# Kernel tuning notes

Hardware: AMD Instinct MI355X
Metric: run time of the kernel (lower is better)

The kernel has to match this reference:

```python
import jax, jax.numpy as jnp
import numpy as np

DIM = 1024
NUM_HEADS = 16
HEAD_DIM = DIM // NUM_HEADS
B, S = 4, 2048


def setup_inputs() -> dict:
    key = jax.random.key(0)
    ks = jax.random.split(key, 6)
    scale = 1.0 / np.sqrt(DIM)
    x = jax.random.normal(ks[0], (B, S, DIM), dtype=jnp.float32)
    # per-head projection weights, torch Linear layout [out, in] stacked over heads
    Wq = jax.random.normal(ks[1], (NUM_HEADS, HEAD_DIM, DIM), dtype=jnp.float32) * scale
    Wk = jax.random.normal(ks[2], (NUM_HEADS, HEAD_DIM, DIM), dtype=jnp.float32) * scale
    Wv = jax.random.normal(ks[3], (NUM_HEADS, HEAD_DIM, DIM), dtype=jnp.float32) * scale
    Wo = jax.random.normal(ks[4], (DIM, DIM), dtype=jnp.float32) * scale
    bo = jax.random.normal(ks[5], (DIM,), dtype=jnp.float32) * scale
    return {"x": x, "Wq": Wq, "Wk": Wk, "Wv": Wv, "Wo": Wo, "bo": bo}


def reference(x, Wq, Wk, Wv, Wo, bo):
    # q/k/v: [B, H, S, E]  (torch Linear: x @ W.T)
    q = jnp.einsum('bsd,hed->bhse', x, Wq)
    k = jnp.einsum('bsd,hed->bhse', x, Wk)
    v = jnp.einsum('bsd,hed->bhse', x, Wv)
    sm_scale = HEAD_DIM ** -0.5
    scores = jnp.einsum('bhse,bhte->bhst', q, k) * sm_scale  # [B,H,S,S]
    attn = jax.nn.softmax(scores, axis=-1)  # dropout is identity (eval)
    out = jnp.einsum('bhst,bhte->bhse', attn, v)  # [B,H,S,E]
    # concat heads (head order matches torch.cat over ModuleList)
    out = out.transpose(0, 2, 1, 3).reshape(B, S, DIM)
    return out @ Wo.T + bo
```

## Files before the change

kernel.cpp:

```cpp
#include <hip/hip_runtime.h>

typedef unsigned short u16;
typedef unsigned int u32;
typedef __attribute__((ext_vector_type(8))) _Float16 f16x8;
typedef __attribute__((ext_vector_type(4))) _Float16 f16x4;
typedef __attribute__((ext_vector_type(8))) unsigned short u16x8;
typedef __attribute__((ext_vector_type(4))) float f32x4;

#define MFMA16(a, b, c) __builtin_amdgcn_mfma_f32_16x16x32_f16(a, b, c, 0, 0, 0)

#define CEXP 0.18033688011112042f

__device__ __forceinline__ void async_copy16(void* lds, const void* gmem) {
  __builtin_amdgcn_global_load_lds((const __attribute__((address_space(1))) u32*)gmem,
                                   (__attribute__((address_space(3))) u32*)lds, 16, 0, 0);
}

__device__ __forceinline__ u32 pack2(float a, float b) {
  return __builtin_bit_cast(u32, __builtin_amdgcn_cvt_pkrtz(a, b));
}

__global__ void cvt_f32_f16(const float* __restrict__ in, _Float16* __restrict__ out, int n4) {
  int i = blockIdx.x * blockDim.x + threadIdx.x;
  if (i < n4) {
    float4 v = ((const float4*)in)[i];
    f16x4 o = {(_Float16)v.x, (_Float16)v.y, (_Float16)v.z, (_Float16)v.w};
    ((f16x4*)out)[i] = o;
  }
}

__global__ void transpose_v(const u16* __restrict__ V, u16* __restrict__ Vt) {
  const int bh = blockIdx.y;
  const int e = threadIdx.x & 63;
  const int sb = threadIdx.x >> 6;
  const int s0 = blockIdx.x * 32 + sb * 8;
  const u16* src = V + ((size_t)bh * 2048 + s0) * 64 + e;
  u16x8 tmp;
#pragma unroll
  for (int j = 0; j < 8; ++j) tmp[j] = src[j * 64];
  u16* dst = Vt + ((size_t)bh * 64 + e) * 2048 + s0;
  *(u16x8*)dst = tmp;
}

template <int EPI>
__global__ void gemm_bt(const _Float16* __restrict__ A, const _Float16* __restrict__ Bt,
                        int M, int N, int K,
                        _Float16* __restrict__ q_out, _Float16* __restrict__ k_out,
                        _Float16* __restrict__ v_out,
                        float* __restrict__ outf, const float* __restrict__ bias) {
  __shared__ _Float16 As[128 * 32];
  __shared__ _Float16 Bs[128 * 32];
  const int tid = threadIdx.x;
  const int lane = tid & 63, wid = tid >> 6;
  const int g = lane >> 4, fr = lane & 15;
  const int wr = wid >> 1, wc = wid & 1;
  const int m0 = blockIdx.y * 128, n0 = blockIdx.x * 128;
  const int ldr = tid >> 2, ldc = (tid & 3) * 8;

  f32x4 acc[4][4];
#pragma unroll
  for (int i = 0; i < 4; ++i)
#pragma unroll
    for (int j = 0; j < 4; ++j) acc[i][j] = (f32x4){0.f, 0.f, 0.f, 0.f};

  const _Float16* ga = A + (size_t)(m0 + ldr) * K + ldc;
  const _Float16* gb = Bt + (size_t)(n0 + ldr) * K + ldc;

  for (int kt = 0; kt < K; kt += 32) {
    __syncthreads();
    async_copy16(&As[(size_t)tid * 8], ga + kt);
    async_copy16(&As[(size_t)(256 + tid) * 8], ga + (size_t)64 * K + kt);
    async_copy16(&Bs[(size_t)tid * 8], gb + kt);
    async_copy16(&Bs[(size_t)(256 + tid) * 8], gb + (size_t)64 * K + kt);
    __syncthreads();
    f16x8 af[4], bf[4];
#pragma unroll
    for (int i = 0; i < 4; ++i) af[i] = *(const f16x8*)&As[(wr * 64 + i * 16 + fr) * 32 + g * 8];
#pragma unroll
    for (int j = 0; j < 4; ++j) bf[j] = *(const f16x8*)&Bs[(wc * 64 + j * 16 + fr) * 32 + g * 8];
#pragma unroll
    for (int i = 0; i < 4; ++i)
#pragma unroll
      for (int j = 0; j < 4; ++j) acc[i][j] = MFMA16(af[i], bf[j], acc[i][j]);
  }

#pragma unroll
  for (int i = 0; i < 4; ++i) {
#pragma unroll
    for (int j = 0; j < 4; ++j) {
      const int rb = m0 + wr * 64 + i * 16 + g * 4;
      const int c = n0 + wc * 64 + j * 16 + fr;
      if (EPI == 0) {
        const int which = c >> 10, nn = c & 1023;
        const int h = nn >> 6, e = nn & 63;
        _Float16* dst = (which == 0) ? q_out : (which == 1) ? k_out : v_out;
#pragma unroll
        for (int r = 0; r < 4; ++r) {
          const int row = rb + r, b = row >> 11, s = row & 2047;
          dst[(((size_t)(b * 16 + h)) * 2048 + s) * 64 + e] = (_Float16)acc[i][j][r];
        }
      } else {
#pragma unroll
        for (int r = 0; r < 4; ++r) {
          const int row = rb + r;
          outf[(size_t)row * N + c] = acc[i][j][r] + bias[c];
        }
      }
    }
  }
}

__global__ __launch_bounds__(256, 4)
void attn_kernel(const _Float16* __restrict__ Q, const _Float16* __restrict__ K,
                 const _Float16* __restrict__ Vt, _Float16* __restrict__ AO) {
  __shared__ _Float16 Ks[64 * 64];
  __shared__ _Float16 Vs[64 * 64];
  const int tid = threadIdx.x;
  const int bh = blockIdx.y;
  const int wid = tid >> 6, lane = tid & 63;
  const int g = lane >> 4, q = lane & 15;
  const int qs = q & 7;

  const int qbase = blockIdx.x * 128 + wid * 32;
  const _Float16* Qp0 = Q + ((size_t)bh * 2048 + qbase + q) * 64;
  f16x8 qf[2][2];
  qf[0][0] = *(const f16x8*)(Qp0 + g * 8);
  qf[0][1] = *(const f16x8*)(Qp0 + 32 + g * 8);
  qf[1][0] = *(const f16x8*)(Qp0 + 16 * 64 + g * 8);
  qf[1][1] = *(const f16x8*)(Qp0 + 16 * 64 + 32 + g * 8);

  const int srow = tid >> 3;
  const int sslot = (tid & 7) ^ (srow & 7);
  const _Float16* ksrc = K + (size_t)bh * 131072 + (size_t)srow * 64 + sslot * 8;
  const _Float16* vsrc = Vt + (size_t)bh * 131072 + (size_t)srow * 2048 + sslot * 8;

  f32x4 o[2][4];
#pragma unroll
  for (int qg = 0; qg < 2; ++qg)
#pragma unroll
    for (int t = 0; t < 4; ++t) o[qg][t] = (f32x4){0.f, 0.f, 0.f, 0.f};
  float m[2] = {-1e30f, -1e30f}, l[2] = {0.f, 0.f};

  for (int s0 = 0; s0 < 2048; s0 += 64) {
    __syncthreads();
    async_copy16(&Ks[(size_t)tid * 8], ksrc + (size_t)s0 * 64);
    async_copy16(&Ks[(size_t)(256 + tid) * 8], ksrc + (size_t)(s0 + 32) * 64);
    async_copy16(&Vs[(size_t)tid * 8], vsrc + s0);
    async_copy16(&Vs[(size_t)(256 + tid) * 8], vsrc + (size_t)32 * 2048 + s0);
    __syncthreads();

    const f32x4 z = {0.f, 0.f, 0.f, 0.f};
    f32x4 st[2][4];
#pragma unroll
    for (int kg = 0; kg < 4; ++kg) {
      const int row = kg * 16 + q;
      const f16x8 ka0 = *(const f16x8*)&Ks[row * 64 + ((g ^ qs) << 3)];
      const f16x8 ka1 = *(const f16x8*)&Ks[row * 64 + ((((g + 4)) ^ qs) << 3)];
      st[0][kg] = MFMA16(ka0, qf[0][0], z);
      st[0][kg] = MFMA16(ka1, qf[0][1], st[0][kg]);
      st[1][kg] = MFMA16(ka0, qf[1][0], z);
      st[1][kg] = MFMA16(ka1, qf[1][1], st[1][kg]);
    }

    u32 pk[2][8];
    float scl[2];
#pragma unroll
    for (int qg = 0; qg < 2; ++qg) {
      float cmax = -1e30f;
#pragma unroll
      for (int kg = 0; kg < 4; ++kg)
#pragma unroll
        for (int r = 0; r < 4; ++r) cmax = fmaxf(cmax, st[qg][kg][r]);
      cmax = fmaxf(cmax, __shfl_xor(cmax, 16));
      cmax = fmaxf(cmax, __shfl_xor(cmax, 32));
      const float mnew = fmaxf(m[qg], cmax);
      scl[qg] = __builtin_amdgcn_exp2f((m[qg] - mnew) * CEXP);
      float psum = 0.f;
#pragma unroll
      for (int kg = 0; kg < 4; ++kg) {
        float p0 = __builtin_amdgcn_exp2f((st[qg][kg][0] - mnew) * CEXP);
        float p1 = __builtin_amdgcn_exp2f((st[qg][kg][1] - mnew) * CEXP);
        float p2 = __builtin_amdgcn_exp2f((st[qg][kg][2] - mnew) * CEXP);
        float p3 = __builtin_amdgcn_exp2f((st[qg][kg][3] - mnew) * CEXP);
        psum += (p0 + p1) + (p2 + p3);
        pk[qg][kg * 2] = pack2(p0, p1);
        pk[qg][kg * 2 + 1] = pack2(p2, p3);
      }
      psum += __shfl_xor(psum, 16);
      psum += __shfl_xor(psum, 32);
      m[qg] = mnew;
      l[qg] = l[qg] * scl[qg] + psum;
    }

    f16x8 vfr[4][2];
#pragma unroll
    for (int t = 0; t < 4; ++t) {
      const int row = t * 16 + q;
      vfr[t][0] = *(const f16x8*)&Vs[row * 64 + ((g ^ qs) << 3)];
      vfr[t][1] = *(const f16x8*)&Vs[row * 64 + (((g + 4) ^ qs) << 3)];
    }

#pragma unroll
    for (int qg = 0; qg < 2; ++qg) {
#pragma unroll
      for (int t = 0; t < 4; ++t) o[qg][t] *= scl[qg];
      union { u32 u[4]; f16x8 v; } pb[2];
#pragma unroll
      for (int sl = 0; sl < 2; ++sl) {
#pragma unroll
        for (int i = 0; i < 4; ++i) {
          const int src = q + 16 * (2 * (g & 1) + (i >> 1));
          const u32 lo = (u32)__shfl((int)pk[qg][sl * 4 + (i & 1)], src, 64);
          const u32 hi = (u32)__shfl((int)pk[qg][sl * 4 + 2 + (i & 1)], src, 64);
          pb[sl].u[i] = (g >> 1) ? hi : lo;
        }
      }
#pragma unroll
      for (int t = 0; t < 4; ++t) {
        o[qg][t] = MFMA16(vfr[t][0], pb[0].v, o[qg][t]);
        o[qg][t] = MFMA16(vfr[t][1], pb[1].v, o[qg][t]);
      }
    }
  }

  const int b = bh >> 4, h = bh & 15;
#pragma unroll
  for (int qg = 0; qg < 2; ++qg) {
    const float inv = 1.0f / l[qg];
    const int qrow = qbase + qg * 16 + q;
    _Float16* dst = AO + ((size_t)(b * 2048 + qrow)) * 1024 + h * 64 + g * 4;
#pragma unroll
    for (int t = 0; t < 4; ++t) {
      f16x4 ov = {(_Float16)(o[qg][t][0] * inv), (_Float16)(o[qg][t][1] * inv),
                  (_Float16)(o[qg][t][2] * inv), (_Float16)(o[qg][t][3] * inv)};
      *(f16x4*)(dst + t * 16) = ov;
    }
  }
}

extern "C" void kernel_launch(void* const* d_in, const int* in_sizes, int n_in,
                              void* d_out, int out_size, void* d_ws, size_t ws_size,
                              hipStream_t stream) {
  const float* x = (const float*)d_in[0];
  const float* Wq = (const float*)d_in[1];
  const float* Wk = (const float*)d_in[2];
  const float* Wv = (const float*)d_in[3];
  const float* Wo = (const float*)d_in[4];
  const float* bo = (const float*)d_in[5];
  float* out = (float*)d_out;

  char* ws = (char*)d_ws;
  _Float16* xb = (_Float16*)(ws);
  _Float16* wqkv = (_Float16*)(ws + 16777216);
  _Float16* wob = (_Float16*)(ws + 23068672);
  _Float16* Qb = (_Float16*)(ws + 25165824);
  _Float16* Kb = (_Float16*)(ws + 41943040);
  _Float16* Vb = (_Float16*)(ws + 58720256);
  _Float16* Vtb = (_Float16*)(ws + 75497472);
  _Float16* AOb = xb;

  cvt_f32_f16<<<8192, 256, 0, stream>>>(x, xb, 2097152);
  cvt_f32_f16<<<1024, 256, 0, stream>>>(Wq, wqkv, 262144);
  cvt_f32_f16<<<1024, 256, 0, stream>>>(Wk, wqkv + 1048576, 262144);
  cvt_f32_f16<<<1024, 256, 0, stream>>>(Wv, wqkv + 2097152, 262144);
  cvt_f32_f16<<<1024, 256, 0, stream>>>(Wo, wob, 262144);

  gemm_bt<0><<<dim3(24, 64), 256, 0, stream>>>(xb, wqkv, 8192, 3072, 1024,
                                               Qb, Kb, Vb, nullptr, nullptr);
  transpose_v<<<dim3(64, 64), 256, 0, stream>>>((const u16*)Vb, (u16*)Vtb);
  attn_kernel<<<dim3(16, 64), 256, 0, stream>>>(Qb, Kb, Vtb, AOb);
  gemm_bt<1><<<dim3(8, 64), 256, 0, stream>>>(AOb, wob, 8192, 1024, 1024,
                                              nullptr, nullptr, nullptr, out, bo);
}
```

Measured before the change: 334.3 us.

## Double-buffer attention K/V, lazy softmax rescale, fuse V transpose and weight casts

```diff
diff --git a/kernel.cpp b/kernel.cpp
--- a/kernel.cpp
+++ b/kernel.cpp
@@ -4,7 +4,6 @@
 typedef unsigned int u32;
 typedef __attribute__((ext_vector_type(8))) _Float16 f16x8;
 typedef __attribute__((ext_vector_type(4))) _Float16 f16x4;
-typedef __attribute__((ext_vector_type(8))) unsigned short u16x8;
 typedef __attribute__((ext_vector_type(4))) float f32x4;
 
 #define MFMA16(a, b, c) __builtin_amdgcn_mfma_f32_16x16x32_f16(a, b, c, 0, 0, 0)
@@ -29,24 +28,23 @@
   }
 }
 
-__global__ void transpose_v(const u16* __restrict__ V, u16* __restrict__ Vt) {
-  const int bh = blockIdx.y;
-  const int e = threadIdx.x & 63;
-  const int sb = threadIdx.x >> 6;
-  const int s0 = blockIdx.x * 32 + sb * 8;
-  const u16* src = V + ((size_t)bh * 2048 + s0) * 64 + e;
-  u16x8 tmp;
-#pragma unroll
-  for (int j = 0; j < 8; ++j) tmp[j] = src[j * 64];
-  u16* dst = Vt + ((size_t)bh * 64 + e) * 2048 + s0;
-  *(u16x8*)dst = tmp;
+__global__ void cvt_weights(const float* __restrict__ Wq, const float* __restrict__ Wk,
+                            const float* __restrict__ Wv, const float* __restrict__ Wo,
+                            _Float16* __restrict__ wqkv, _Float16* __restrict__ wob) {
+  const int i = blockIdx.x * blockDim.x + threadIdx.x;
+  const int wsel = i >> 18, off = i & 262143;
+  const float* src = (wsel == 0) ? Wq : (wsel == 1) ? Wk : (wsel == 2) ? Wv : Wo;
+  float4 v = ((const float4*)src)[off];
+  f16x4 o = {(_Float16)v.x, (_Float16)v.y, (_Float16)v.z, (_Float16)v.w};
+  if (wsel < 3) ((f16x4*)wqkv)[i] = o;
+  else ((f16x4*)wob)[off] = o;
 }
 
 template <int EPI>
 __global__ void gemm_bt(const _Float16* __restrict__ A, const _Float16* __restrict__ Bt,
                         int M, int N, int K,
                         _Float16* __restrict__ q_out, _Float16* __restrict__ k_out,
-                        _Float16* __restrict__ v_out,
+                        _Float16* __restrict__ vt_out,
                         float* __restrict__ outf, const float* __restrict__ bias) {
   __shared__ _Float16 As[128 * 32];
   __shared__ _Float16 Bs[128 * 32];
@@ -78,10 +76,12 @@
     for (int i = 0; i < 4; ++i) af[i] = *(const f16x8*)&As[(wr * 64 + i * 16 + fr) * 32 + g * 8];
 #pragma unroll
     for (int j = 0; j < 4; ++j) bf[j] = *(const f16x8*)&Bs[(wc * 64 + j * 16 + fr) * 32 + g * 8];
+    __builtin_amdgcn_s_setprio(1);
 #pragma unroll
     for (int i = 0; i < 4; ++i)
 #pragma unroll
       for (int j = 0; j < 4; ++j) acc[i][j] = MFMA16(af[i], bf[j], acc[i][j]);
+    __builtin_amdgcn_s_setprio(0);
   }
 
 #pragma unroll
@@ -93,11 +93,18 @@
       if (EPI == 0) {
         const int which = c >> 10, nn = c & 1023;
         const int h = nn >> 6, e = nn & 63;
-        _Float16* dst = (which == 0) ? q_out : (which == 1) ? k_out : v_out;
-#pragma unroll
-        for (int r = 0; r < 4; ++r) {
-          const int row = rb + r, b = row >> 11, s = row & 2047;
-          dst[(((size_t)(b * 16 + h)) * 2048 + s) * 64 + e] = (_Float16)acc[i][j][r];
+        if (which == 2) {
+          const int b = rb >> 11, s = rb & 2047;
+          f16x4 ov = {(_Float16)acc[i][j][0], (_Float16)acc[i][j][1],
+                      (_Float16)acc[i][j][2], (_Float16)acc[i][j][3]};
+          *(f16x4*)&vt_out[((size_t)((b * 16 + h) * 64 + e)) * 2048 + s] = ov;
+        } else {
+          _Float16* dst = (which == 0) ? q_out : k_out;
+#pragma unroll
+          for (int r = 0; r < 4; ++r) {
+            const int row = rb + r, b = row >> 11, s = row & 2047;
+            dst[(((size_t)(b * 16 + h)) * 2048 + s) * 64 + e] = (_Float16)acc[i][j][r];
+          }
         }
       } else {
 #pragma unroll
@@ -113,8 +120,8 @@
 __global__ __launch_bounds__(256, 4)
 void attn_kernel(const _Float16* __restrict__ Q, const _Float16* __restrict__ K,
                  const _Float16* __restrict__ Vt, _Float16* __restrict__ AO) {
-  __shared__ _Float16 Ks[64 * 64];
-  __shared__ _Float16 Vs[64 * 64];
+  __shared__ _Float16 Ks[2][64 * 64];
+  __shared__ _Float16 Vs[2][64 * 64];
   const int tid = threadIdx.x;
   const int bh = blockIdx.y;
   const int wid = tid >> 6, lane = tid & 63;
@@ -134,36 +141,48 @@
   const _Float16* ksrc = K + (size_t)bh * 131072 + (size_t)srow * 64 + sslot * 8;
   const _Float16* vsrc = Vt + (size_t)bh * 131072 + (size_t)srow * 2048 + sslot * 8;
 
+#define STAGE(buf, s0)                                                        \
+  do {                                                                        \
+    async_copy16(&Ks[buf][(size_t)tid * 8], ksrc + (size_t)(s0) * 64);        \
+    async_copy16(&Ks[buf][(size_t)(256 + tid) * 8],                           \
+                 ksrc + (size_t)((s0) + 32) * 64);                            \
+    async_copy16(&Vs[buf][(size_t)tid * 8], vsrc + (s0));                     \
+    async_copy16(&Vs[buf][(size_t)(256 + tid) * 8],                           \
+                 vsrc + (size_t)32 * 2048 + (s0));                            \
+  } while (0)
+
   f32x4 o[2][4];
 #pragma unroll
   for (int qg = 0; qg < 2; ++qg)
 #pragma unroll
-    for (int t = 0; t < 4; ++t) o[qg][t] = (f32x4){0.f, 0.f, 0.f, 0.f};
+    for (int u = 0; u < 4; ++u) o[qg][u] = (f32x4){0.f, 0.f, 0.f, 0.f};
   float m[2] = {-1e30f, -1e30f}, l[2] = {0.f, 0.f};
 
-  for (int s0 = 0; s0 < 2048; s0 += 64) {
-    __syncthreads();
-    async_copy16(&Ks[(size_t)tid * 8], ksrc + (size_t)s0 * 64);
-    async_copy16(&Ks[(size_t)(256 + tid) * 8], ksrc + (size_t)(s0 + 32) * 64);
-    async_copy16(&Vs[(size_t)tid * 8], vsrc + s0);
-    async_copy16(&Vs[(size_t)(256 + tid) * 8], vsrc + (size_t)32 * 2048 + s0);
-    __syncthreads();
+  STAGE(0, 0);
+  __syncthreads();
+
+  for (int it = 0; it < 32; ++it) {
+    const int cur = it & 1;
+    if (it < 31) STAGE(cur ^ 1, (it + 1) * 64);
+    const _Float16* Kc = Ks[cur];
+    const _Float16* Vc = Vs[cur];
 
     const f32x4 z = {0.f, 0.f, 0.f, 0.f};
     f32x4 st[2][4];
 #pragma unroll
     for (int kg = 0; kg < 4; ++kg) {
       const int row = kg * 16 + q;
-      const f16x8 ka0 = *(const f16x8*)&Ks[row * 64 + ((g ^ qs) << 3)];
-      const f16x8 ka1 = *(const f16x8*)&Ks[row * 64 + ((((g + 4)) ^ qs) << 3)];
+      const f16x8 ka0 = *(const f16x8*)&Kc[row * 64 + ((g ^ qs) << 3)];
+      const f16x8 ka1 = *(const f16x8*)&Kc[row * 64 + (((g + 4) ^ qs) << 3)];
+      __builtin_amdgcn_s_setprio(1);
       st[0][kg] = MFMA16(ka0, qf[0][0], z);
       st[0][kg] = MFMA16(ka1, qf[0][1], st[0][kg]);
       st[1][kg] = MFMA16(ka0, qf[1][0], z);
       st[1][kg] = MFMA16(ka1, qf[1][1], st[1][kg]);
+      __builtin_amdgcn_s_setprio(0);
     }
 
     u32 pk[2][8];
-    float scl[2];
 #pragma unroll
     for (int qg = 0; qg < 2; ++qg) {
       float cmax = -1e30f;
@@ -173,37 +192,42 @@
         for (int r = 0; r < 4; ++r) cmax = fmaxf(cmax, st[qg][kg][r]);
       cmax = fmaxf(cmax, __shfl_xor(cmax, 16));
       cmax = fmaxf(cmax, __shfl_xor(cmax, 32));
-      const float mnew = fmaxf(m[qg], cmax);
-      scl[qg] = __builtin_amdgcn_exp2f((m[qg] - mnew) * CEXP);
+      const float mq = m[qg];
+      if (!__all(cmax <= mq + 8.0f)) {
+        const float mnew = fmaxf(mq, cmax);
+        const float scl = __builtin_amdgcn_exp2f((mq - mnew) * CEXP);
+#pragma unroll
+        for (int u = 0; u < 4; ++u) o[qg][u] *= scl;
+        l[qg] *= scl;
+        m[qg] = mnew;
+      }
+      const float mcur = m[qg];
       float psum = 0.f;
 #pragma unroll
       for (int kg = 0; kg < 4; ++kg) {
-        float p0 = __builtin_amdgcn_exp2f((st[qg][kg][0] - mnew) * CEXP);
-        float p1 = __builtin_amdgcn_exp2f((st[qg][kg][1] - mnew) * CEXP);
-        float p2 = __builtin_amdgcn_exp2f((st[qg][kg][2] - mnew) * CEXP);
-        float p3 = __builtin_amdgcn_exp2f((st[qg][kg][3] - mnew) * CEXP);
+        float p0 = __builtin_amdgcn_exp2f((st[qg][kg][0] - mcur) * CEXP);
+        float p1 = __builtin_amdgcn_exp2f((st[qg][kg][1] - mcur) * CEXP);
+        float p2 = __builtin_amdgcn_exp2f((st[qg][kg][2] - mcur) * CEXP);
+        float p3 = __builtin_amdgcn_exp2f((st[qg][kg][3] - mcur) * CEXP);
         psum += (p0 + p1) + (p2 + p3);
         pk[qg][kg * 2] = pack2(p0, p1);
         pk[qg][kg * 2 + 1] = pack2(p2, p3);
       }
       psum += __shfl_xor(psum, 16);
       psum += __shfl_xor(psum, 32);
-      m[qg] = mnew;
-      l[qg] = l[qg] * scl[qg] + psum;
+      l[qg] += psum;
     }
 
     f16x8 vfr[4][2];
 #pragma unroll
-    for (int t = 0; t < 4; ++t) {
-      const int row = t * 16 + q;
-      vfr[t][0] = *(const f16x8*)&Vs[row * 64 + ((g ^ qs) << 3)];
-      vfr[t][1] = *(const f16x8*)&Vs[row * 64 + (((g + 4) ^ qs) << 3)];
+    for (int t4 = 0; t4 < 4; ++t4) {
+      const int row = t4 * 16 + q;
+      vfr[t4][0] = *(const f16x8*)&Vc[row * 64 + ((g ^ qs) << 3)];
+      vfr[t4][1] = *(const f16x8*)&Vc[row * 64 + (((g + 4) ^ qs) << 3)];
     }
 
 #pragma unroll
     for (int qg = 0; qg < 2; ++qg) {
-#pragma unroll
-      for (int t = 0; t < 4; ++t) o[qg][t] *= scl[qg];
       union { u32 u[4]; f16x8 v; } pb[2];
 #pragma unroll
       for (int sl = 0; sl < 2; ++sl) {
@@ -215,12 +239,15 @@
           pb[sl].u[i] = (g >> 1) ? hi : lo;
         }
       }
-#pragma unroll
-      for (int t = 0; t < 4; ++t) {
-        o[qg][t] = MFMA16(vfr[t][0], pb[0].v, o[qg][t]);
-        o[qg][t] = MFMA16(vfr[t][1], pb[1].v, o[qg][t]);
-      }
-    }
+      __builtin_amdgcn_s_setprio(1);
+#pragma unroll
+      for (int t4 = 0; t4 < 4; ++t4) {
+        o[qg][t4] = MFMA16(vfr[t4][0], pb[0].v, o[qg][t4]);
+        o[qg][t4] = MFMA16(vfr[t4][1], pb[1].v, o[qg][t4]);
+      }
+      __builtin_amdgcn_s_setprio(0);
+    }
+    __syncthreads();
   }
 
   const int b = bh >> 4, h = bh & 15;
@@ -230,12 +257,13 @@
     const int qrow = qbase + qg * 16 + q;
     _Float16* dst = AO + ((size_t)(b * 2048 + qrow)) * 1024 + h * 64 + g * 4;
 #pragma unroll
-    for (int t = 0; t < 4; ++t) {
-      f16x4 ov = {(_Float16)(o[qg][t][0] * inv), (_Float16)(o[qg][t][1] * inv),
-                  (_Float16)(o[qg][t][2] * inv), (_Float16)(o[qg][t][3] * inv)};
-      *(f16x4*)(dst + t * 16) = ov;
-    }
-  }
+    for (int t4 = 0; t4 < 4; ++t4) {
+      f16x4 ov = {(_Float16)(o[qg][t4][0] * inv), (_Float16)(o[qg][t4][1] * inv),
+                  (_Float16)(o[qg][t4][2] * inv), (_Float16)(o[qg][t4][3] * inv)};
+      *(f16x4*)(dst + t4 * 16) = ov;
+    }
+  }
+#undef STAGE
 }
 
 extern "C" void kernel_launch(void* const* d_in, const int* in_sizes, int n_in,
@@ -255,19 +283,14 @@
   _Float16* wob = (_Float16*)(ws + 23068672);
   _Float16* Qb = (_Float16*)(ws + 25165824);
   _Float16* Kb = (_Float16*)(ws + 41943040);
-  _Float16* Vb = (_Float16*)(ws + 58720256);
-  _Float16* Vtb = (_Float16*)(ws + 75497472);
+  _Float16* Vtb = (_Float16*)(ws + 58720256);
   _Float16* AOb = xb;
 
   cvt_f32_f16<<<8192, 256, 0, stream>>>(x, xb, 2097152);
-  cvt_f32_f16<<<1024, 256, 0, stream>>>(Wq, wqkv, 262144);
-  cvt_f32_f16<<<1024, 256, 0, stream>>>(Wk, wqkv + 1048576, 262144);
-  cvt_f32_f16<<<1024, 256, 0, stream>>>(Wv, wqkv + 2097152, 262144);
-  cvt_f32_f16<<<1024, 256, 0, stream>>>(Wo, wob, 262144);
+  cvt_weights<<<4096, 256, 0, stream>>>(Wq, Wk, Wv, Wo, wqkv, wob);
 
   gemm_bt<0><<<dim3(24, 64), 256, 0, stream>>>(xb, wqkv, 8192, 3072, 1024,
-                                               Qb, Kb, Vb, nullptr, nullptr);
-  transpose_v<<<dim3(64, 64), 256, 0, stream>>>((const u16*)Vb, (u16*)Vtb);
+                                               Qb, Kb, Vtb, nullptr, nullptr);
   attn_kernel<<<dim3(16, 64), 256, 0, stream>>>(Qb, Kb, Vtb, AOb);
   gemm_bt<1><<<dim3(8, 64), 256, 0, stream>>>(AOb, wob, 8192, 1024, 1024,
                                               nullptr, nullptr, nullptr, out, bo);
```

Result: faster. 313.1 us (-6.3%).
